# Kernel optimization log

Hardware: AMD Instinct MI355X
Metric: run time of the kernel (lower is better)

Reference implementation:

```python
import jax, jax.numpy as jnp
import numpy as np
from jax import lax


def bilinear_resize(x, oh, ow):
    # x: (..., H, W); torch F.interpolate bilinear, align_corners=False
    H, W = x.shape[-2], x.shape[-1]
    def coords(n_in, n_out):
        src = (jnp.arange(n_out, dtype=jnp.float32) + 0.5) * (n_in / n_out) - 0.5
        src = jnp.clip(src, 0.0, n_in - 1.0)
        i0 = jnp.floor(src).astype(jnp.int32)
        i1 = jnp.minimum(i0 + 1, n_in - 1)
        return i0, i1, src - i0.astype(jnp.float32)
    r0, r1, wr = coords(H, oh)
    c0, c1, wc = coords(W, ow)
    xr = x[..., r0, :] * (1.0 - wr)[:, None] + x[..., r1, :] * wr[:, None]
    return xr[..., c0] * (1.0 - wc) + xr[..., c1] * wc


def setup_inputs():
    key = jax.random.key(0)
    ks = jax.random.split(key, 20)
    B, D, C, WIN, NH, A = 256, 1280, 64, 14, 8, 49
    def p(k, *sh):
        return jax.random.normal(k, sh, dtype=jnp.float32) * 0.02
    return {
        "X": jax.random.normal(ks[0], (B, 3, D), dtype=jnp.float32),
        "W_embed": p(ks[1], C * WIN * WIN, D), "b_embed": p(ks[2], C * WIN * WIN),
        "W_qkv": p(ks[3], 3 * C, C),
        "W_proj": p(ks[4], C, C), "b_proj": p(ks[5], C),
        "dwc_w": p(ks[6], C, 1, 3, 3), "dwc_b": p(ks[7], C),
        "an_bias": p(ks[8], NH, A, 7, 7), "na_bias": p(ks[9], NH, A, 7, 7),
        "ah_bias": p(ks[10], 1, NH, A, WIN, 1), "aw_bias": p(ks[11], 1, NH, A, 1, WIN),
        "ha_bias": p(ks[12], 1, NH, WIN, 1, A), "wa_bias": p(ks[13], 1, NH, 1, WIN, A),
        "W_adj": p(ks[14], 256, C * WIN * WIN), "b_adj": p(ks[15], 256),
        "W_t1": p(ks[16], 256, D), "b_t1": p(ks[17], 256),
        "W_t2": p(ks[18], 128, 256), "b_t2": p(ks[19], 128),
    }


def reference(X, W_embed, b_embed, W_qkv, W_proj, b_proj, dwc_w, dwc_b,
              an_bias, na_bias, ah_bias, aw_bias, ha_bias, wa_bias,
              W_adj, b_adj, W_t1, b_t1, W_t2, b_t2):
    B = X.shape[0]
    C, WIN, NH, A = 64, 14, 8, 49
    N = WIN * WIN            # 196 tokens
    HD = C // NH             # head dim 8
    scale = HD ** -0.5
    b3 = 3 * B

    # embed_to_img: (B*3, 1280) -> (B*3, C*N) -> tokens (B*3, N, C)
    Xe = X.reshape(b3, -1) @ W_embed.T + b_embed
    xt = Xe.reshape(b3, N, C)

    # AgentAttention
    qkv = xt @ W_qkv.T                                  # (b3, N, 3C), qkv_bias=False
    q, k, v = jnp.split(qkv, 3, axis=-1)
    # agent tokens: AdaptiveAvgPool2d 14x14 -> 7x7 over q (exact 2x2 mean)
    agent = q.reshape(b3, 7, 2, 7, 2, C).mean(axis=(2, 4)).reshape(b3, A, C)
    q = q.reshape(b3, N, NH, HD).transpose(0, 2, 1, 3)
    k = k.reshape(b3, N, NH, HD).transpose(0, 2, 1, 3)
    v = v.reshape(b3, N, NH, HD).transpose(0, 2, 1, 3)
    agent = agent.reshape(b3, A, NH, HD).transpose(0, 2, 1, 3)

    # stage 1: agents attend to all tokens
    pb = bilinear_resize(an_bias, WIN, WIN).reshape(NH, A, N) \
         + (ah_bias + aw_bias).reshape(NH, A, N)
    agent_attn = jax.nn.softmax(jnp.einsum('bhad,bhnd->bhan', agent * scale, k) + pb, axis=-1)
    agent_v = jnp.einsum('bhan,bhnd->bhad', agent_attn, v)   # (b3, NH, A, HD)

    # stage 2: tokens attend to agents
    ab = bilinear_resize(na_bias, WIN, WIN).reshape(NH, A, N).transpose(0, 2, 1) \
         + (ha_bias + wa_bias).reshape(NH, N, A)
    q_attn = jax.nn.softmax(jnp.einsum('bhnd,bhad->bhna', q * scale, agent) + ab, axis=-1)
    o = jnp.einsum('bhna,bhad->bhnd', q_attn, agent_v)
    o = o.transpose(0, 2, 1, 3).reshape(b3, N, C)

    # depthwise conv enhancement on v
    v_img = v.transpose(0, 2, 1, 3).reshape(b3, WIN, WIN, C).transpose(0, 3, 1, 2)
    dwc = lax.conv_general_dilated(v_img, dwc_w, (1, 1), [(1, 1), (1, 1)],
                                   feature_group_count=C) + dwc_b[None, :, None, None]
    o = o + dwc.transpose(0, 2, 3, 1).reshape(b3, N, C)
    o = o @ W_proj.T + b_proj

    X_adj = (o.reshape(b3, -1) @ W_adj.T + b_adj).reshape(B, 3, -1)

    def mlp(z):
        return jnp.tanh(z @ W_t1.T + b_t1) @ W_t2.T + b_t2
    anchor, pos, neg = mlp(X[:, 0]), mlp(X[:, 1]), mlp(X[:, 2])
    return anchor, pos, neg, X_adj
```

## Files before the change

### kernel.cpp

```cpp
#include <hip/hip_runtime.h>

using u16 = unsigned short;
using u32 = unsigned int;

constexpr int Bn   = 256;
constexpr int Dd   = 1280;
constexpr int Cc   = 64;
constexpr int WINc = 14;
constexpr int NHc  = 8;
constexpr int Ac   = 49;
constexpr int Nc   = WINc * WINc;
constexpr int HDc  = Cc / NHc;
constexpr int B3c  = 3 * Bn;
constexpr int CNc  = Cc * Nc;

typedef __attribute__((ext_vector_type(8))) short v8s;
typedef __attribute__((ext_vector_type(4))) float v4f;
typedef __attribute__((ext_vector_type(2))) float v2f;

__device__ __forceinline__ float bflo(u32 u){ union{u32 x; float f;} c; c.x = u << 16; return c.f; }
__device__ __forceinline__ float bfhi(u32 u){ union{u32 x; float f;} c; c.x = u & 0xffff0000u; return c.f; }
__device__ __forceinline__ float bfs(u16 h){ union{u32 x; float f;} c; c.x = ((u32)h) << 16; return c.f; }
__device__ __forceinline__ u16 f2bb(float f){
  u32 u = __float_as_uint(f);
  u32 r = (u + 0x7fffu + ((u >> 16) & 1u)) >> 16;
  return (u16)r;
}
__device__ __forceinline__ void unpack8(uint4 u, float* dst){
  dst[0]=bflo(u.x); dst[1]=bfhi(u.x); dst[2]=bflo(u.y); dst[3]=bfhi(u.y);
  dst[4]=bflo(u.z); dst[5]=bfhi(u.z); dst[6]=bflo(u.w); dst[7]=bfhi(u.w);
}
__device__ __forceinline__ uint4 pack8(const float* s){
  uint4 r;
  r.x = (u32)f2bb(s[0]) | ((u32)f2bb(s[1]) << 16);
  r.y = (u32)f2bb(s[2]) | ((u32)f2bb(s[3]) << 16);
  r.z = (u32)f2bb(s[4]) | ((u32)f2bb(s[5]) << 16);
  r.w = (u32)f2bb(s[6]) | ((u32)f2bb(s[7]) << 16);
  return r;
}

__device__ __forceinline__ void gl_lds16(const u16* g, u16* l){
  __builtin_amdgcn_global_load_lds(
      (const __attribute__((address_space(1))) unsigned int*)g,
      (__attribute__((address_space(3))) unsigned int*)l,
      16, 0, 0);
}

constexpr int WeN   = 12544 * 1280;
constexpr int XN    = 768 * 1280;
constexpr int WadjN = 256 * CNc;
constexpr int W1N   = 256 * 1280;
constexpr int W2N   = 128 * 256;
__global__ __launch_bounds__(256) void conv_bf16_kernel(const float* __restrict__ We,
                                                        const float* __restrict__ X,
                                                        const float* __restrict__ Wadj,
                                                        const float* __restrict__ W1,
                                                        const float* __restrict__ W2,
                                                        u16* __restrict__ WeB,
                                                        u16* __restrict__ XB,
                                                        u16* __restrict__ WadjB,
                                                        u16* __restrict__ W1B,
                                                        u16* __restrict__ W2B)
{
  const size_t idx = ((size_t)blockIdx.x * 256 + threadIdx.x) * 8;
  const float* src; u16* dst;
  if (idx < (size_t)WeN)                          { src = We + idx;                         dst = WeB + idx; }
  else if (idx < (size_t)WeN + XN)                { src = X + (idx - WeN);                  dst = XB + (idx - WeN); }
  else if (idx < (size_t)WeN + XN + WadjN)        { src = Wadj + (idx - WeN - XN);          dst = WadjB + (idx - WeN - XN); }
  else if (idx < (size_t)WeN + XN + WadjN + W1N)  { src = W1 + (idx - WeN - XN - WadjN);    dst = W1B + (idx - WeN - XN - WadjN); }
  else                                            { src = W2 + (idx - WeN - XN - WadjN - W1N); dst = W2B + (idx - WeN - XN - WadjN - W1N); }
  float v[8];
  *reinterpret_cast<float4*>(&v[0]) = *reinterpret_cast<const float4*>(src);
  *reinterpret_cast<float4*>(&v[4]) = *reinterpret_cast<const float4*>(src + 4);
  *reinterpret_cast<uint4*>(dst) = pack8(v);
}

template<int KK, int NN, bool TANH>
__global__ __launch_bounds__(256) void gemm_bf16_t(const u16* __restrict__ Amat,
                                                   const u16* __restrict__ Bmat,
                                                   const float* __restrict__ bias,
                                                   u16* __restrict__ Cmat)
{
  __shared__ u16 As[128 * 32];
  __shared__ u16 Bs[128 * 32];
  const int t = threadIdx.x;
  const int n0 = blockIdx.x * 128, m0 = blockIdx.y * 128;
  const int wave = t >> 6, lane = t & 63;
  const int wm = wave >> 1, wn = wave & 1;
  const int mi = lane & 15, quad = lane >> 4;

  v4f acc[4][4];
  #pragma unroll
  for (int a = 0; a < 4; ++a)
    #pragma unroll
    for (int b = 0; b < 4; ++b) acc[a][b] = (v4f){0.f, 0.f, 0.f, 0.f};

  const int rs = wave*32 + (lane >> 2);
  const int cs = (lane & 3) * 8;
  const u16* ga0 = Amat + (size_t)(m0 + rs) * KK + cs;
  const u16* ga1 = Amat + (size_t)(m0 + rs + 16) * KK + cs;
  const u16* gb0 = Bmat + (size_t)(n0 + rs) * KK + cs;
  const u16* gb1 = Bmat + (size_t)(n0 + rs + 16) * KK + cs;
  u16* la0 = &As[(wave*32)      * 32];
  u16* la1 = &As[(wave*32 + 16) * 32];
  u16* lb0 = &Bs[(wave*32)      * 32];
  u16* lb1 = &Bs[(wave*32 + 16) * 32];

  for (int kt = 0; kt < KK; kt += 32) {
    gl_lds16(ga0 + kt, la0);
    gl_lds16(ga1 + kt, la1);
    gl_lds16(gb0 + kt, lb0);
    gl_lds16(gb1 + kt, lb1);
    __syncthreads();

    v8s af[4], bf[4];
    #pragma unroll
    for (int mt = 0; mt < 4; ++mt)
      af[mt] = *reinterpret_cast<const v8s*>(&As[(wm*64 + mt*16 + mi)*32 + quad*8]);
    #pragma unroll
    for (int nt = 0; nt < 4; ++nt)
      bf[nt] = *reinterpret_cast<const v8s*>(&Bs[(wn*64 + nt*16 + mi)*32 + quad*8]);
    #pragma unroll
    for (int mt = 0; mt < 4; ++mt)
      #pragma unroll
      for (int nt = 0; nt < 4; ++nt)
        acc[mt][nt] = __builtin_amdgcn_mfma_f32_16x16x32_bf16(af[mt], bf[nt], acc[mt][nt], 0, 0, 0);
    __syncthreads();
  }

  #pragma unroll
  for (int nt = 0; nt < 4; ++nt) {
    const int col = n0 + wn*64 + nt*16 + mi;
    const float bc = bias[col];
    #pragma unroll
    for (int mt = 0; mt < 4; ++mt) {
      #pragma unroll
      for (int r = 0; r < 4; ++r) {
        const int row = m0 + wm*64 + mt*16 + quad*4 + r;
        float val = acc[mt][nt][r] + bc;
        if constexpr (TANH) val = tanhf(val);
        Cmat[(size_t)row * NN + col] = f2bb(val);
      }
    }
  }
}

__global__ __launch_bounds__(256) void mlp2_mfma(const u16* __restrict__ H,
                                                 const u16* __restrict__ W2B,
                                                 const float* __restrict__ b2,
                                                 float* __restrict__ outp)
{
  __shared__ u16 As[128 * 40];
  __shared__ u16 Bs[128 * 40];
  const int t = threadIdx.x;
  const int m0 = blockIdx.x * 128;
  const int wave = t >> 6, lane = t & 63;
  const int wm = wave >> 1, wn = wave & 1;
  const int mi = lane & 15, quad = lane >> 4;
  const int srow = t >> 1, scol = (t & 1) * 16;

  v4f acc[4][4];
  #pragma unroll
  for (int a = 0; a < 4; ++a)
    #pragma unroll
    for (int b = 0; b < 4; ++b) acc[a][b] = (v4f){0.f, 0.f, 0.f, 0.f};

  for (int kt = 0; kt < 256; kt += 32) {
    const u16* ap = H + (size_t)(m0 + srow) * 256 + kt + scol;
    *reinterpret_cast<uint4*>(&As[srow*40 + scol])     = *reinterpret_cast<const uint4*>(ap);
    *reinterpret_cast<uint4*>(&As[srow*40 + scol + 8]) = *reinterpret_cast<const uint4*>(ap + 8);
    const u16* bp = W2B + (size_t)srow * 256 + kt + scol;
    *reinterpret_cast<uint4*>(&Bs[srow*40 + scol])     = *reinterpret_cast<const uint4*>(bp);
    *reinterpret_cast<uint4*>(&Bs[srow*40 + scol + 8]) = *reinterpret_cast<const uint4*>(bp + 8);
    __syncthreads();

    v8s af[4], bf[4];
    #pragma unroll
    for (int mt = 0; mt < 4; ++mt)
      af[mt] = *reinterpret_cast<const v8s*>(&As[(wm*64 + mt*16 + mi)*40 + quad*8]);
    #pragma unroll
    for (int nt = 0; nt < 4; ++nt)
      bf[nt] = *reinterpret_cast<const v8s*>(&Bs[(wn*64 + nt*16 + mi)*40 + quad*8]);
    #pragma unroll
    for (int mt = 0; mt < 4; ++mt)
      #pragma unroll
      for (int nt = 0; nt < 4; ++nt)
        acc[mt][nt] = __builtin_amdgcn_mfma_f32_16x16x32_bf16(af[mt], bf[nt], acc[mt][nt], 0, 0, 0);
    __syncthreads();
  }

  #pragma unroll
  for (int nt = 0; nt < 4; ++nt) {
    const int col = wn*64 + nt*16 + mi;
    const float bc = b2[col];
    #pragma unroll
    for (int mt = 0; mt < 4; ++mt) {
      #pragma unroll
      for (int r = 0; r < 4; ++r) {
        const int row = m0 + wm*64 + mt*16 + quad*4 + r;
        const int bi = row / 3, s = row - bi * 3;
        outp[(size_t)s * (Bn*128) + (size_t)bi * 128 + col] = acc[mt][nt][r] + bc;
      }
    }
  }
}

__global__ __launch_bounds__(256) void qkv_mfma(const u16* __restrict__ xt, const float* __restrict__ Wqkv,
                                                u16* __restrict__ qh, u16* __restrict__ kh, u16* __restrict__ vb)
{
  __shared__ u16 As[256 * 72];
  __shared__ u16 Bs[64 * 72];
  const int t = threadIdx.x;
  const int m0 = blockIdx.x * 256;
  const int seg = blockIdx.y;
  const int wave = t >> 6, lane = t & 63;
  const int mi = lane & 15, quad = lane >> 4;

  for (int i = t; i < Cc*Cc; i += 256) {
    const int j = i >> 6, c = i & 63;
    Bs[j*72 + c] = f2bb(Wqkv[(size_t)(seg*64 + j)*64 + c]);
  }
  {
    const int ar = t >> 2, ac = (t & 3) * 16;
    #pragma unroll
    for (int rb = 0; rb < 4; ++rb) {
      const int row = rb*64 + ar;
      const uint4* src = reinterpret_cast<const uint4*>(xt + ((size_t)(m0 + row))*64 + ac);
      *reinterpret_cast<uint4*>(&As[row*72 + ac])     = src[0];
      *reinterpret_cast<uint4*>(&As[row*72 + ac + 8]) = src[1];
    }
  }
  __syncthreads();

  v4f acc[4][4];
  #pragma unroll
  for (int a = 0; a < 4; ++a)
    #pragma unroll
    for (int b = 0; b < 4; ++b) acc[a][b] = (v4f){0.f, 0.f, 0.f, 0.f};

  #pragma unroll
  for (int ks = 0; ks < 2; ++ks) {
    v8s af[4], bf[4];
    #pragma unroll
    for (int mt = 0; mt < 4; ++mt)
      af[mt] = *reinterpret_cast<const v8s*>(&As[(wave*64 + mt*16 + mi)*72 + ks*32 + quad*8]);
    #pragma unroll
    for (int nt = 0; nt < 4; ++nt)
      bf[nt] = *reinterpret_cast<const v8s*>(&Bs[(nt*16 + mi)*72 + ks*32 + quad*8]);
    #pragma unroll
    for (int mt = 0; mt < 4; ++mt)
      #pragma unroll
      for (int nt = 0; nt < 4; ++nt)
        acc[mt][nt] = __builtin_amdgcn_mfma_f32_16x16x32_bf16(af[mt], bf[nt], acc[mt][nt], 0, 0, 0);
  }

  u16* hm = (seg == 0) ? qh : kh;
  #pragma unroll
  for (int nt = 0; nt < 4; ++nt) {
    const int col = nt*16 + mi;
    const int h = col >> 3, d = col & 7;
    #pragma unroll
    for (int mt = 0; mt < 4; ++mt) {
      #pragma unroll
      for (int r = 0; r < 4; ++r) {
        const int row = m0 + wave*64 + mt*16 + quad*4 + r;
        const u16 val = f2bb(acc[mt][nt][r]);
        if (seg < 2) {
          const int b = row / Nc, n = row - b * Nc;
          hm[((size_t)(b*NHc + h)*Nc + n)*8 + d] = val;
        } else {
          vb[(size_t)row * 64 + col] = val;
        }
      }
    }
  }
}

__global__ __launch_bounds__(256) void bias_kernel(const float* __restrict__ an, const float* __restrict__ na,
                                                   const float* __restrict__ ah, const float* __restrict__ aw,
                                                   const float* __restrict__ ha, const float* __restrict__ wa,
                                                   float* __restrict__ pb, float* __restrict__ ab)
{
  const int total = NHc * Ac * Nc;
  int idx = blockIdx.x * 256 + threadIdx.x;
  if (idx >= 2 * total) return;
  const bool isab = idx >= total;
  const int r = isab ? idx - total : idx;
  const int h = r / (Ac * Nc);
  const int r2 = r % (Ac * Nc);
  int a, n;
  if (isab) { n = r2 / Ac; a = r2 % Ac; } else { a = r2 / Nc; n = r2 % Nc; }
  const int y = n / WINc, x = n % WINc;
  float sy = fminf(fmaxf(0.5f * y - 0.25f, 0.f), 6.f);
  float sx = fminf(fmaxf(0.5f * x - 0.25f, 0.f), 6.f);
  const int y0 = (int)sy, x0 = (int)sx;
  const float wy = sy - y0, wx = sx - x0;
  const int y1 = (y0 + 1 < 6) ? y0 + 1 : 6;
  const int x1 = (x0 + 1 < 6) ? x0 + 1 : 6;
  const float* src = (isab ? na : an) + (h * Ac + a) * 49;
  const float v00 = src[y0*7 + x0], v01 = src[y0*7 + x1];
  const float v10 = src[y1*7 + x0], v11 = src[y1*7 + x1];
  const float bi = (1.f - wy) * ((1.f - wx) * v00 + wx * v01)
                 + wy * ((1.f - wx) * v10 + wx * v11);
  if (!isab) pb[((size_t)h*Nc + n)*Ac + a] = bi + ah[(h*Ac + a)*WINc + y] + aw[(h*Ac + a)*WINc + x];
  else       ab[((size_t)h*Ac + a)*Nc + n] = bi + ha[(h*WINc + y)*Ac + a] + wa[(h*WINc + x)*Ac + a];
}

__global__ __launch_bounds__(256) void attn_kernel(const u16* __restrict__ qh, const u16* __restrict__ kh,
                                                   const u16* __restrict__ v,
                                                   const float* __restrict__ pb, const float* __restrict__ ab,
                                                   u16* __restrict__ o)
{
  __shared__ float sU[Nc*10];
  __shared__ float sK[Nc*8], sV[Nc*8];
  __shared__ float sAg[Ac*8], sAV[Ac*8];
  const int bh = blockIdx.x;
  const int b = bh >> 3, h = bh & 7;
  const int t = threadIdx.x;
  const float scale = 0.3535533905932738f;

  float qreg[8];
  if (t < Nc) {
    const size_t base = ((size_t)bh * Nc + t) * 8;
    unpack8(*reinterpret_cast<const uint4*>(qh + base), qreg);
    #pragma unroll
    for (int d = 0; d < 8; ++d) sU[t*8 + d] = qreg[d];
    unpack8(*reinterpret_cast<const uint4*>(kh + base), &sK[t*8]);
    unpack8(*reinterpret_cast<const uint4*>(v + ((size_t)b*Nc + t)*64 + h*8), &sV[t*8]);
  }
  __syncthreads();

  for (int i = t; i < Ac*8; i += 256) {
    const int a = i >> 3, d = i & 7;
    const int ay = a / 7, ax = a % 7;
    const int n00 = (ay * 2) * WINc + ax * 2;
    sAg[i] = 0.25f * (sU[n00*8+d] + sU[(n00+1)*8+d] + sU[(n00+WINc)*8+d] + sU[(n00+WINc+1)*8+d]);
  }
  __syncthreads();

  if (t < Nc) {
    const int qd = t / Ac, a = t - qd * Ac;
    const int nb = qd * Ac;
    v2f g2[4];
    #pragma unroll
    for (int d2 = 0; d2 < 4; ++d2) g2[d2] = *reinterpret_cast<const v2f*>(&sAg[a*8 + d2*2]);
    const float* pbr = pb + ((size_t)h*Nc + nb)*Ac + a;
    float l0 = 0.f, l1 = 0.f;
    v2f avA[4] = {}, avB[4] = {};
    for (int j = 0; j < 48; j += 2) {
      const v2f* k0 = reinterpret_cast<const v2f*>(&sK[(nb + j)*8]);
      const v2f* k1 = reinterpret_cast<const v2f*>(&sK[(nb + j + 1)*8]);
      v2f sa = (g2[0]*k0[0] + g2[1]*k0[1]) + (g2[2]*k0[2] + g2[3]*k0[3]);
      v2f sb = (g2[0]*k1[0] + g2[1]*k1[1]) + (g2[2]*k1[2] + g2[3]*k1[3]);
      const float e0 = __expf((sa.x + sa.y) * scale + pbr[j*Ac]);
      const float e1 = __expf((sb.x + sb.y) * scale + pbr[(j+1)*Ac]);
      l0 += e0; l1 += e1;
      const v2f* v0 = reinterpret_cast<const v2f*>(&sV[(nb + j)*8]);
      const v2f* v1 = reinterpret_cast<const v2f*>(&sV[(nb + j + 1)*8]);
      const v2f e02 = {e0, e0}, e12 = {e1, e1};
      #pragma unroll
      for (int d2 = 0; d2 < 4; ++d2) { avA[d2] += e02 * v0[d2]; avB[d2] += e12 * v1[d2]; }
    }
    {
      const v2f* k0 = reinterpret_cast<const v2f*>(&sK[(nb + 48)*8]);
      v2f sa = (g2[0]*k0[0] + g2[1]*k0[1]) + (g2[2]*k0[2] + g2[3]*k0[3]);
      const float e0 = __expf((sa.x + sa.y) * scale + pbr[48*Ac]);
      l0 += e0;
      const v2f* v0 = reinterpret_cast<const v2f*>(&sV[(nb + 48)*8]);
      const v2f e02 = {e0, e0};
      #pragma unroll
      for (int d2 = 0; d2 < 4; ++d2) avA[d2] += e02 * v0[d2];
    }
    float* pp = &sU[t*9];
    pp[0] = l0 + l1;
    #pragma unroll
    for (int d2 = 0; d2 < 4; ++d2) {
      const v2f m = avA[d2] + avB[d2];
      pp[1+d2*2] = m.x; pp[2+d2*2] = m.y;
    }
  }
  __syncthreads();

  if (t < Ac) {
    float L = 0.f, av[8] = {};
    #pragma unroll
    for (int p = 0; p < 4; ++p) {
      const float* pp = &sU[(p*Ac + t)*9];
      L += pp[0];
      #pragma unroll
      for (int d = 0; d < 8; ++d) av[d] += pp[1+d];
    }
    const float inv = 1.f / L;
    #pragma unroll
    for (int d = 0; d < 8; ++d) sAV[t*8 + d] = av[d] * inv;
  }
  __syncthreads();

  if (t < Nc) {
    v2f q2[4];
    #pragma unroll
    for (int d2 = 0; d2 < 4; ++d2) q2[d2] = (v2f){qreg[d2*2], qreg[d2*2+1]};
    const float* abr = ab + (size_t)h*Ac*Nc + t;
    float l0 = 0.f, l1 = 0.f;
    v2f oA[4] = {}, oB[4] = {};
    for (int a = 0; a < 48; a += 2) {
      const v2f* g0 = reinterpret_cast<const v2f*>(&sAg[a*8]);
      const v2f* g1 = reinterpret_cast<const v2f*>(&sAg[(a+1)*8]);
      v2f sa = (q2[0]*g0[0] + q2[1]*g0[1]) + (q2[2]*g0[2] + q2[3]*g0[3]);
      v2f sb = (q2[0]*g1[0] + q2[1]*g1[1]) + (q2[2]*g1[2] + q2[3]*g1[3]);
      const float e0 = __expf((sa.x + sa.y) * scale + abr[a*Nc]);
      const float e1 = __expf((sb.x + sb.y) * scale + abr[(a+1)*Nc]);
      l0 += e0; l1 += e1;
      const v2f* a0 = reinterpret_cast<const v2f*>(&sAV[a*8]);
      const v2f* a1 = reinterpret_cast<const v2f*>(&sAV[(a+1)*8]);
      const v2f e02 = {e0, e0}, e12 = {e1, e1};
      #pragma unroll
      for (int d2 = 0; d2 < 4; ++d2) { oA[d2] += e02 * a0[d2]; oB[d2] += e12 * a1[d2]; }
    }
    {
      const v2f* g0 = reinterpret_cast<const v2f*>(&sAg[48*8]);
      v2f sa = (q2[0]*g0[0] + q2[1]*g0[1]) + (q2[2]*g0[2] + q2[3]*g0[3]);
      const float e0 = __expf((sa.x + sa.y) * scale + abr[48*Nc]);
      l0 += e0;
      const v2f* a0 = reinterpret_cast<const v2f*>(&sAV[48*8]);
      const v2f e02 = {e0, e0};
      #pragma unroll
      for (int d2 = 0; d2 < 4; ++d2) oA[d2] += e02 * a0[d2];
    }
    const float inv = 1.f / (l0 + l1);
    float o8[8];
    #pragma unroll
    for (int d2 = 0; d2 < 4; ++d2) {
      const v2f m = oA[d2] + oB[d2];
      o8[d2*2] = m.x * inv; o8[d2*2+1] = m.y * inv;
    }
    *reinterpret_cast<uint4*>(&o[((size_t)b*Nc + t)*64 + h*8]) = pack8(o8);
  }
}

__global__ __launch_bounds__(256) void dwc_kernel(const u16* __restrict__ o, const u16* __restrict__ v,
                                                  const float* __restrict__ dwc_w, const float* __restrict__ dwc_b,
                                                  u16* __restrict__ U)
{
  __shared__ u16 sV[Nc*Cc];
  const int b = blockIdx.x, t = threadIdx.x;

  const uint2* vsrc = reinterpret_cast<const uint2*>(v + (size_t)b * CNc);
  uint2* sV2 = reinterpret_cast<uint2*>(sV);
  for (int i = t; i < CNc/4; i += 256) sV2[i] = vsrc[i];
  __syncthreads();

  const u16* ob = o + (size_t)b * CNc;
  u16* ub = U + (size_t)b * CNc;
  for (int i = t; i < CNc; i += 256) {
    const int n = i >> 6, c = i & 63;
    const int y = n / WINc, x = n % WINc;
    float acc = dwc_b[c] + bfs(ob[i]);
    #pragma unroll
    for (int ky = 0; ky < 3; ++ky) {
      const int yy = y + ky - 1;
      if (yy < 0 || yy >= WINc) continue;
      #pragma unroll
      for (int kx = 0; kx < 3; ++kx) {
        const int xx = x + kx - 1;
        if (xx < 0 || xx >= WINc) continue;
        acc = fmaf(dwc_w[c*9 + ky*3 + kx], bfs(sV[(yy*WINc + xx)*Cc + c]), acc);
      }
    }
    ub[i] = f2bb(acc);
  }
}

__global__ __launch_bounds__(256) void proj_mfma(const u16* __restrict__ U,
                                                 const float* __restrict__ Wp,
                                                 const float* __restrict__ bp,
                                                 u16* __restrict__ oproj)
{
  __shared__ u16 As[256 * 72];
  __shared__ u16 Bs[64 * 72];
  const int t = threadIdx.x;
  const int m0 = blockIdx.x * 256;
  const int wave = t >> 6, lane = t & 63;
  const int mi = lane & 15, quad = lane >> 4;

  for (int i = t; i < Cc*Cc; i += 256) {
    const int j = i >> 6, c = i & 63;
    Bs[j*72 + c] = f2bb(Wp[i]);
  }
  {
    const int ar = t >> 2, ac = (t & 3) * 16;
    #pragma unroll
    for (int rb = 0; rb < 4; ++rb) {
      const int row = rb*64 + ar;
      const uint4* src = reinterpret_cast<const uint4*>(U + ((size_t)(m0 + row))*64 + ac);
      *reinterpret_cast<uint4*>(&As[row*72 + ac])     = src[0];
      *reinterpret_cast<uint4*>(&As[row*72 + ac + 8]) = src[1];
    }
  }
  __syncthreads();

  v4f acc[4][4];
  #pragma unroll
  for (int a = 0; a < 4; ++a)
    #pragma unroll
    for (int b = 0; b < 4; ++b) acc[a][b] = (v4f){0.f, 0.f, 0.f, 0.f};

  #pragma unroll
  for (int ks = 0; ks < 2; ++ks) {
    v8s af[4], bf[4];
    #pragma unroll
    for (int mt = 0; mt < 4; ++mt)
      af[mt] = *reinterpret_cast<const v8s*>(&As[(wave*64 + mt*16 + mi)*72 + ks*32 + quad*8]);
    #pragma unroll
    for (int nt = 0; nt < 4; ++nt)
      bf[nt] = *reinterpret_cast<const v8s*>(&Bs[(nt*16 + mi)*72 + ks*32 + quad*8]);
    #pragma unroll
    for (int mt = 0; mt < 4; ++mt)
      #pragma unroll
      for (int nt = 0; nt < 4; ++nt)
        acc[mt][nt] = __builtin_amdgcn_mfma_f32_16x16x32_bf16(af[mt], bf[nt], acc[mt][nt], 0, 0, 0);
  }

  #pragma unroll
  for (int nt = 0; nt < 4; ++nt) {
    const int col = nt*16 + mi;
    const float bc = bp[col];
    #pragma unroll
    for (int mt = 0; mt < 4; ++mt) {
      #pragma unroll
      for (int r = 0; r < 4; ++r) {
        const int row = m0 + wave*64 + mt*16 + quad*4 + r;
        oproj[(size_t)row * 64 + col] = f2bb(acc[mt][nt][r] + bc);
      }
    }
  }
}

__global__ __launch_bounds__(256) void gemm_adj_mfma(const u16* __restrict__ Amat,
                                                     const u16* __restrict__ BmatB,
                                                     float* __restrict__ part)
{
  constexpr int K = CNc, Kc = CNc/8;
  __shared__ u16 As[128 * 32];
  __shared__ u16 Bs[128 * 32];
  const int t = threadIdx.x;
  const int n0 = blockIdx.x * 128, m0 = blockIdx.y * 128;
  const int kbeg = blockIdx.z * Kc;
  const int wave = t >> 6, lane = t & 63;
  const int wm = wave >> 1, wn = wave & 1;
  const int mi = lane & 15, quad = lane >> 4;

  v4f acc[4][4];
  #pragma unroll
  for (int a = 0; a < 4; ++a)
    #pragma unroll
    for (int b = 0; b < 4; ++b) acc[a][b] = (v4f){0.f, 0.f, 0.f, 0.f};

  const int rs = wave*32 + (lane >> 2);
  const int cs = (lane & 3) * 8;
  const u16* ga0 = Amat + (size_t)(m0 + rs) * K + kbeg + cs;
  const u16* ga1 = Amat + (size_t)(m0 + rs + 16) * K + kbeg + cs;
  const u16* gb0 = BmatB + (size_t)(n0 + rs) * K + kbeg + cs;
  const u16* gb1 = BmatB + (size_t)(n0 + rs + 16) * K + kbeg + cs;
  u16* la0 = &As[(wave*32)      * 32];
  u16* la1 = &As[(wave*32 + 16) * 32];
  u16* lb0 = &Bs[(wave*32)      * 32];
  u16* lb1 = &Bs[(wave*32 + 16) * 32];

  for (int kt = 0; kt < Kc; kt += 32) {
    gl_lds16(ga0 + kt, la0);
    gl_lds16(ga1 + kt, la1);
    gl_lds16(gb0 + kt, lb0);
    gl_lds16(gb1 + kt, lb1);
    __syncthreads();

    v8s af[4], bf[4];
    #pragma unroll
    for (int mt = 0; mt < 4; ++mt)
      af[mt] = *reinterpret_cast<const v8s*>(&As[(wm*64 + mt*16 + mi)*32 + quad*8]);
    #pragma unroll
    for (int nt = 0; nt < 4; ++nt)
      bf[nt] = *reinterpret_cast<const v8s*>(&Bs[(wn*64 + nt*16 + mi)*32 + quad*8]);
    #pragma unroll
    for (int mt = 0; mt < 4; ++mt)
      #pragma unroll
      for (int nt = 0; nt < 4; ++nt)
        acc[mt][nt] = __builtin_amdgcn_mfma_f32_16x16x32_bf16(af[mt], bf[nt], acc[mt][nt], 0, 0, 0);
    __syncthreads();
  }

  const size_t zoff = (size_t)blockIdx.z * B3c * 256;
  #pragma unroll
  for (int nt = 0; nt < 4; ++nt) {
    const int col = n0 + wn*64 + nt*16 + mi;
    #pragma unroll
    for (int mt = 0; mt < 4; ++mt) {
      #pragma unroll
      for (int r = 0; r < 4; ++r) {
        const int row = m0 + wm*64 + mt*16 + quad*4 + r;
        part[zoff + (size_t)row * 256 + col] = acc[mt][nt][r];
      }
    }
  }
}

__global__ __launch_bounds__(256) void reduce_bias_kernel(const float* __restrict__ part,
                                                          const float* __restrict__ bias,
                                                          float* __restrict__ outp)
{
  const int idx = blockIdx.x * 256 + threadIdx.x;
  const int n = idx & 255;
  float acc = bias[n];
  #pragma unroll
  for (int s = 0; s < 8; ++s) acc += part[(size_t)s * B3c * 256 + idx];
  outp[idx] = acc;
}

extern "C" void kernel_launch(void* const* d_in, const int* in_sizes, int n_in,
                              void* d_out, int out_size, void* d_ws, size_t ws_size,
                              hipStream_t stream)
{
  auto in = [&](int i){ return reinterpret_cast<const float*>(d_in[i]); };
  const float *X = in(0), *We = in(1), *be = in(2), *Wq = in(3), *Wp = in(4), *bp = in(5),
              *dww = in(6), *dwb = in(7), *anb = in(8), *nab = in(9), *ahb = in(10), *awb = in(11),
              *hab = in(12), *wab = in(13), *Wadj = in(14), *badj = in(15),
              *W1 = in(16), *b1 = in(17), *W2 = in(18), *b2 = in(19);
  float* out = reinterpret_cast<float*>(d_out);
  char* w = reinterpret_cast<char*>(d_ws);

  const size_t TOK = (size_t)B3c * CNc;
  u16* xt = reinterpret_cast<u16*>(w);
  u16* qh = reinterpret_cast<u16*>(w + TOK*2);
  u16* kh = reinterpret_cast<u16*>(w + TOK*4);
  u16* vb = reinterpret_cast<u16*>(w + TOK*6);
  float* pb = reinterpret_cast<float*>(w + TOK*8);
  float* ab = pb + NHc*Ac*Nc;
  u16* WadjB = reinterpret_cast<u16*>(ab + NHc*Ac*Nc);
  u16* XB  = WadjB + WadjN;
  u16* W1B = XB + XN;
  u16* W2B = W1B + W1N;
  u16* H   = W2B + W2N;
  u16* WeB = qh;
  u16* U = qh;
  float* part = reinterpret_cast<float*>(kh);

  conv_bf16_kernel<<<dim3((WeN + XN + WadjN + W1N + W2N)/(256*8)), 256, 0, stream>>>(
      We, X, Wadj, W1, W2, WeB, XB, WadjB, W1B, W2B);
  gemm_bf16_t<Dd, CNc, false><<<dim3(CNc/128, B3c/128), 256, 0, stream>>>(XB, WeB, be, xt);
  qkv_mfma<<<dim3((B3c*Nc)/256, 3), 256, 0, stream>>>(xt, Wq, qh, kh, vb);
  bias_kernel<<<dim3((2*NHc*Ac*Nc + 255)/256), 256, 0, stream>>>(anb, nab, ahb, awb, hab, wab, pb, ab);
  attn_kernel<<<dim3(B3c*NHc), 256, 0, stream>>>(qh, kh, vb, pb, ab, xt );
  dwc_kernel<<<dim3(B3c), 256, 0, stream>>>(xt , vb, dww, dwb, U);
  proj_mfma<<<dim3((B3c*Nc)/256), 256, 0, stream>>>(U, Wp, bp, xt );
  gemm_adj_mfma<<<dim3(256/128, B3c/128, 8), 256, 0, stream>>>(xt , WadjB, part);
  reduce_bias_kernel<<<dim3((B3c*256)/256), 256, 0, stream>>>(part, badj, out + 3*Bn*128);
  gemm_bf16_t<Dd, 256, true><<<dim3(256/128, B3c/128), 256, 0, stream>>>(XB, W1B, b1, H);
  mlp2_mfma<<<dim3(B3c/128), 256, 0, stream>>>(H, W2B, b2, out);
}
```

Before: 501.3 us.

## Remap embed GEMM blocks across XCDs and fuse two-layer MLP into one kernel

The embed GEMM now remaps each flat workgroup id so that consecutive tiles, which share operand rows, land on the same XCD and get better L2 reuse. The two MLP GEMMs are fused into one kernel that keeps the tanh hidden layer in shared memory instead of writing it to global memory and launching a second kernel. The fused kernel uses only 6 blocks and runs both hidden-layer column chunks serially, so it has very little parallelism. The MLP is a small part of total time.

```diff
diff --git a/kernel.cpp b/kernel.cpp
--- a/kernel.cpp
+++ b/kernel.cpp
@@ -75,16 +75,24 @@
   *reinterpret_cast<uint4*>(dst) = pack8(v);
 }
 
-template<int KK, int NN, bool TANH>
-__global__ __launch_bounds__(256) void gemm_bf16_t(const u16* __restrict__ Amat,
-                                                   const u16* __restrict__ Bmat,
-                                                   const float* __restrict__ bias,
-                                                   u16* __restrict__ Cmat)
-{
+__global__ __launch_bounds__(256) void gemm_embed_bf16(const u16* __restrict__ Amat,
+                                                       const u16* __restrict__ Bmat,
+                                                       const float* __restrict__ bias,
+                                                       u16* __restrict__ Cmat)
+{
+  constexpr int K = Dd, Nn = CNc;
   __shared__ u16 As[128 * 32];
   __shared__ u16 Bs[128 * 32];
   const int t = threadIdx.x;
-  const int n0 = blockIdx.x * 128, m0 = blockIdx.y * 128;
+
+  const int nwg = gridDim.x * gridDim.y;
+  const int flat = blockIdx.y * gridDim.x + blockIdx.x;
+  const int q = nwg >> 3, r = nwg & 7;
+  const int xcd = flat & 7, p = flat >> 3;
+  const int wgid = xcd * q + (xcd < r ? xcd : r) + p;
+  const int n0 = (wgid / gridDim.y) * 128;
+  const int m0 = (wgid % gridDim.y) * 128;
+
   const int wave = t >> 6, lane = t & 63;
   const int wm = wave >> 1, wn = wave & 1;
   const int mi = lane & 15, quad = lane >> 4;
@@ -97,16 +105,16 @@
 
   const int rs = wave*32 + (lane >> 2);
   const int cs = (lane & 3) * 8;
-  const u16* ga0 = Amat + (size_t)(m0 + rs) * KK + cs;
-  const u16* ga1 = Amat + (size_t)(m0 + rs + 16) * KK + cs;
-  const u16* gb0 = Bmat + (size_t)(n0 + rs) * KK + cs;
-  const u16* gb1 = Bmat + (size_t)(n0 + rs + 16) * KK + cs;
+  const u16* ga0 = Amat + (size_t)(m0 + rs) * K + cs;
+  const u16* ga1 = Amat + (size_t)(m0 + rs + 16) * K + cs;
+  const u16* gb0 = Bmat + (size_t)(n0 + rs) * K + cs;
+  const u16* gb1 = Bmat + (size_t)(n0 + rs + 16) * K + cs;
   u16* la0 = &As[(wave*32)      * 32];
   u16* la1 = &As[(wave*32 + 16) * 32];
   u16* lb0 = &Bs[(wave*32)      * 32];
   u16* lb1 = &Bs[(wave*32 + 16) * 32];
 
-  for (int kt = 0; kt < KK; kt += 32) {
+  for (int kt = 0; kt < K; kt += 32) {
     gl_lds16(ga0 + kt, la0);
     gl_lds16(ga1 + kt, la1);
     gl_lds16(gb0 + kt, lb0);
@@ -135,29 +143,88 @@
     #pragma unroll
     for (int mt = 0; mt < 4; ++mt) {
       #pragma unroll
-      for (int r = 0; r < 4; ++r) {
-        const int row = m0 + wm*64 + mt*16 + quad*4 + r;
-        float val = acc[mt][nt][r] + bc;
-        if constexpr (TANH) val = tanhf(val);
-        Cmat[(size_t)row * NN + col] = f2bb(val);
+      for (int r2 = 0; r2 < 4; ++r2) {
+        const int row = m0 + wm*64 + mt*16 + quad*4 + r2;
+        Cmat[(size_t)row * Nn + col] = f2bb(acc[mt][nt][r2] + bc);
       }
     }
   }
 }
 
-__global__ __launch_bounds__(256) void mlp2_mfma(const u16* __restrict__ H,
+__global__ __launch_bounds__(256) void mlp_fused(const u16* __restrict__ XB,
+                                                 const u16* __restrict__ W1B,
                                                  const u16* __restrict__ W2B,
+                                                 const float* __restrict__ b1,
                                                  const float* __restrict__ b2,
                                                  float* __restrict__ outp)
 {
-  __shared__ u16 As[128 * 40];
-  __shared__ u16 Bs[128 * 40];
+  __shared__ u16 As[128 * 32];
+  __shared__ u16 Bs[128 * 32];
+  __shared__ u16 sH[128 * 264];
   const int t = threadIdx.x;
   const int m0 = blockIdx.x * 128;
   const int wave = t >> 6, lane = t & 63;
   const int wm = wave >> 1, wn = wave & 1;
   const int mi = lane & 15, quad = lane >> 4;
-  const int srow = t >> 1, scol = (t & 1) * 16;
+
+  const int rs = wave*32 + (lane >> 2);
+  const int cs = (lane & 3) * 8;
+  u16* la0 = &As[(wave*32)      * 32];
+  u16* la1 = &As[(wave*32 + 16) * 32];
+  u16* lb0 = &Bs[(wave*32)      * 32];
+  u16* lb1 = &Bs[(wave*32 + 16) * 32];
+
+  const u16* ga0 = XB + (size_t)(m0 + rs) * Dd + cs;
+  const u16* ga1 = XB + (size_t)(m0 + rs + 16) * Dd + cs;
+
+  for (int nc = 0; nc < 2; ++nc) {
+    const int n0 = nc * 128;
+    const u16* gb0 = W1B + (size_t)(n0 + rs) * Dd + cs;
+    const u16* gb1 = W1B + (size_t)(n0 + rs + 16) * Dd + cs;
+
+    v4f acc[4][4];
+    #pragma unroll
+    for (int a = 0; a < 4; ++a)
+      #pragma unroll
+      for (int b = 0; b < 4; ++b) acc[a][b] = (v4f){0.f, 0.f, 0.f, 0.f};
+
+    for (int kt = 0; kt < Dd; kt += 32) {
+      gl_lds16(ga0 + kt, la0);
+      gl_lds16(ga1 + kt, la1);
+      gl_lds16(gb0 + kt, lb0);
+      gl_lds16(gb1 + kt, lb1);
+      __syncthreads();
+
+      v8s af[4], bf[4];
+      #pragma unroll
+      for (int mt = 0; mt < 4; ++mt)
+        af[mt] = *reinterpret_cast<const v8s*>(&As[(wm*64 + mt*16 + mi)*32 + quad*8]);
+      #pragma unroll
+      for (int nt = 0; nt < 4; ++nt)
+        bf[nt] = *reinterpret_cast<const v8s*>(&Bs[(wn*64 + nt*16 + mi)*32 + quad*8]);
+      #pragma unroll
+      for (int mt = 0; mt < 4; ++mt)
+        #pragma unroll
+        for (int nt = 0; nt < 4; ++nt)
+          acc[mt][nt] = __builtin_amdgcn_mfma_f32_16x16x32_bf16(af[mt], bf[nt], acc[mt][nt], 0, 0, 0);
+      __syncthreads();
+    }
+
+    #pragma unroll
+    for (int nt = 0; nt < 4; ++nt) {
+      const int col = n0 + wn*64 + nt*16 + mi;
+      const float bc = b1[col];
+      #pragma unroll
+      for (int mt = 0; mt < 4; ++mt) {
+        #pragma unroll
+        for (int r = 0; r < 4; ++r) {
+          const int rowl = wm*64 + mt*16 + quad*4 + r;
+          sH[rowl*264 + col] = f2bb(tanhf(acc[mt][nt][r] + bc));
+        }
+      }
+    }
+    __syncthreads();
+  }
 
   v4f acc[4][4];
   #pragma unroll
@@ -165,22 +232,21 @@
     #pragma unroll
     for (int b = 0; b < 4; ++b) acc[a][b] = (v4f){0.f, 0.f, 0.f, 0.f};
 
+  const u16* gb0 = W2B + (size_t)rs * 256 + cs;
+  const u16* gb1 = W2B + (size_t)(rs + 16) * 256 + cs;
+
   for (int kt = 0; kt < 256; kt += 32) {
-    const u16* ap = H + (size_t)(m0 + srow) * 256 + kt + scol;
-    *reinterpret_cast<uint4*>(&As[srow*40 + scol])     = *reinterpret_cast<const uint4*>(ap);
-    *reinterpret_cast<uint4*>(&As[srow*40 + scol + 8]) = *reinterpret_cast<const uint4*>(ap + 8);
-    const u16* bp = W2B + (size_t)srow * 256 + kt + scol;
-    *reinterpret_cast<uint4*>(&Bs[srow*40 + scol])     = *reinterpret_cast<const uint4*>(bp);
-    *reinterpret_cast<uint4*>(&Bs[srow*40 + scol + 8]) = *reinterpret_cast<const uint4*>(bp + 8);
+    gl_lds16(gb0 + kt, lb0);
+    gl_lds16(gb1 + kt, lb1);
     __syncthreads();
 
     v8s af[4], bf[4];
     #pragma unroll
     for (int mt = 0; mt < 4; ++mt)
-      af[mt] = *reinterpret_cast<const v8s*>(&As[(wm*64 + mt*16 + mi)*40 + quad*8]);
+      af[mt] = *reinterpret_cast<const v8s*>(&sH[(wm*64 + mt*16 + mi)*264 + kt + quad*8]);
     #pragma unroll
     for (int nt = 0; nt < 4; ++nt)
-      bf[nt] = *reinterpret_cast<const v8s*>(&Bs[(wn*64 + nt*16 + mi)*40 + quad*8]);
+      bf[nt] = *reinterpret_cast<const v8s*>(&Bs[(wn*64 + nt*16 + mi)*32 + quad*8]);
     #pragma unroll
     for (int mt = 0; mt < 4; ++mt)
       #pragma unroll
@@ -639,14 +705,13 @@
   u16* XB  = WadjB + WadjN;
   u16* W1B = XB + XN;
   u16* W2B = W1B + W1N;
-  u16* H   = W2B + W2N;
   u16* WeB = qh;
   u16* U = qh;
   float* part = reinterpret_cast<float*>(kh);
 
   conv_bf16_kernel<<<dim3((WeN + XN + WadjN + W1N + W2N)/(256*8)), 256, 0, stream>>>(
       We, X, Wadj, W1, W2, WeB, XB, WadjB, W1B, W2B);
-  gemm_bf16_t<Dd, CNc, false><<<dim3(CNc/128, B3c/128), 256, 0, stream>>>(XB, WeB, be, xt);
+  gemm_embed_bf16<<<dim3(CNc/128, B3c/128), 256, 0, stream>>>(XB, WeB, be, xt);
   qkv_mfma<<<dim3((B3c*Nc)/256, 3), 256, 0, stream>>>(xt, Wq, qh, kh, vb);
   bias_kernel<<<dim3((2*NHc*Ac*Nc + 255)/256), 256, 0, stream>>>(anb, nab, ahb, awb, hab, wab, pb, ab);
   attn_kernel<<<dim3(B3c*NHc), 256, 0, stream>>>(qh, kh, vb, pb, ab, xt );
@@ -654,6 +719,5 @@
   proj_mfma<<<dim3((B3c*Nc)/256), 256, 0, stream>>>(U, Wp, bp, xt );
   gemm_adj_mfma<<<dim3(256/128, B3c/128, 8), 256, 0, stream>>>(xt , WadjB, part);
   reduce_bias_kernel<<<dim3((B3c*256)/256), 256, 0, stream>>>(part, badj, out + 3*Bn*128);
-  gemm_bf16_t<Dd, 256, true><<<dim3(256/128, B3c/128), 256, 0, stream>>>(XB, W1B, b1, H);
-  mlp2_mfma<<<dim3(B3c/128), 256, 0, stream>>>(H, W2B, b2, out);
-}
+  mlp_fused<<<dim3(B3c/128), 256, 0, stream>>>(XB, W1B, W2B, b1, b2, out);
+}
```

New measurement: 530.4 us. 1.06x slower.
